# Kernel optimization log

Hardware: AMD Instinct MI355X
Metric: run time of the kernel (lower is better)

## Reference

```python
import jax, jax.numpy as jnp
import numpy as np

N = 100_000      # nodes
E = 1_600_000    # edges (avg degree 16)
F_IN = 128       # dataset.num_features
H = 128          # hidden
C = 25_000       # num_clusters (~ target_ratio 0.25 * N)
G = 64           # graphs in batch
NCLS = 10        # dataset.num_classes


def _gcn_conv(x, w, b, src, dst, n):
    # PyG GCNConv: add self loops, symmetric normalization deg^-1/2 A_hat deg^-1/2
    h = x @ w  # [n, out]
    deg = jnp.zeros((n,), x.dtype).at[dst].add(1.0) + 1.0  # +1 self loop
    dis = jax.lax.rsqrt(deg)
    norm = dis[src] * dis[dst]  # [E]
    out = jnp.zeros_like(h).at[dst].add(h[src] * norm[:, None])
    out = out + h * (dis * dis)[:, None]  # self-loop term norm_ii = deg_i^-1
    return out + b


def _mean_pool(x, seg, num_seg):
    s = jax.ops.segment_sum(x, seg, num_segments=num_seg)
    cnt = jax.ops.segment_sum(jnp.ones((x.shape[0],), x.dtype), seg, num_segments=num_seg)
    return s / jnp.maximum(cnt, 1.0)[:, None]


def _max_pool(x, seg, num_seg):
    m = jax.ops.segment_max(x, seg, num_segments=num_seg)
    cnt = jax.ops.segment_sum(jnp.ones((x.shape[0],), x.dtype), seg, num_segments=num_seg)
    return jnp.where(cnt[:, None] > 0, m, 0.0)


def setup_inputs() -> dict:
    key = jax.random.key(0)
    ks = jax.random.split(key, 12)
    def glorot(k, shape):
        fan_in = shape[0]
        return (jax.random.normal(k, shape, jnp.float32) / np.sqrt(fan_in)).astype(jnp.float32)
    return {
        "x": jax.random.normal(ks[0], (N, F_IN), jnp.float32),
        "edge_index": jax.random.randint(ks[1], (2, E), 0, N, dtype=jnp.int32).astype(jnp.int64),
        "batch": jnp.sort(jax.random.randint(ks[2], (N,), 0, G, dtype=jnp.int32)).astype(jnp.int64),
        "cluster": jax.random.randint(ks[3], (N,), 0, C, dtype=jnp.int32).astype(jnp.int64),
        "num_clusters": C,
        "num_graphs": G,
        "W1": glorot(ks[4], (F_IN, H)), "b1": jnp.zeros((H,), jnp.float32),
        "W2": glorot(ks[5], (H, H)),   "b2": jnp.zeros((H,), jnp.float32),
        "W3": glorot(ks[6], (H, H)),   "b3": jnp.zeros((H,), jnp.float32),
        "lin1_w": glorot(ks[7], (4 * H, H)), "lin1_b": jnp.zeros((H,), jnp.float32),
        "lin2_w": glorot(ks[8], (H, NCLS)),  "lin2_b": jnp.zeros((NCLS,), jnp.float32),
    }


def reference(x, edge_index, batch, cluster, num_clusters, num_graphs,
              W1, b1, W2, b2, W3, b3, lin1_w, lin1_b, lin2_w, lin2_b):
    n = x.shape[0]
    src, dst = edge_index[0], edge_index[1]
    # conv1 + relu (dropout is identity in eval mode)
    h = jax.nn.relu(_gcn_conv(x, W1, b1, src, dst, n))
    pre_mean = _mean_pool(h, batch, num_graphs)
    pre_max = _max_pool(h, batch, num_graphs)
    # LaCorePooling(aggregate='mean'): segment-mean nodes by cluster id,
    # relabel edges to cluster ids, derive pooled batch vector.
    hp = _mean_pool(h, cluster, num_clusters)            # [C, H]
    src_p, dst_p = cluster[src], cluster[dst]            # pooled edge list
    batch_p = jax.ops.segment_max(batch, cluster, num_segments=num_clusters)
    batch_p = jnp.maximum(batch_p, 0)                    # empty clusters -> graph 0
    # post-pool GCN layers
    hp = jax.nn.relu(_gcn_conv(hp, W2, b2, src_p, dst_p, num_clusters))
    hp = jax.nn.relu(_gcn_conv(hp, W3, b3, src_p, dst_p, num_clusters))
    post_mean = _mean_pool(hp, batch_p, num_graphs)
    post_max = _max_pool(hp, batch_p, num_graphs)
    z = jnp.concatenate([pre_mean, pre_max, post_mean, post_max], axis=-1)  # [G, 4H]
    z = jax.nn.relu(z @ lin1_w + lin1_b)
    z = z @ lin2_w + lin2_b
    return jax.nn.log_softmax(z, axis=-1)
```

## Files before the change

### kernel.cpp

```cpp
#include <hip/hip_runtime.h>

constexpr int N_NODES = 100000;
constexpr int N_EDGES = 1600000;
constexpr int N_CLUST = 25000;
constexpr int N_GRAPH = 64;
constexpr int NCLSN   = 10;

constexpr int BKT1_SHIFT = 9;
constexpr int NBKT1 = (N_NODES + 511) / 512;
constexpr int EPB = 4096;
constexpr int NEB = (N_EDGES + EPB - 1) / EPB;
constexpr int SORT_CAP = 12288;

constexpr int SCAN_BPB = 1024;
constexpr int NB1 = (N_NODES + SCAN_BPB - 1) / SCAN_BPB;
constexpr int NB2 = (N_CLUST + SCAN_BPB - 1) / SCAN_BPB;
constexpr int NB3 = (N_CLUST + SCAN_BPB - 1) / SCAN_BPB;
constexpr int NBT = NB1 + NB2 + NB3;

__device__ __forceinline__ float bf16lo(unsigned u){ return __uint_as_float(u << 16); }
__device__ __forceinline__ float bf16hi(unsigned u){ return __uint_as_float(u & 0xffff0000u); }
__device__ __forceinline__ unsigned bf16_rne(float f){
  unsigned u = __float_as_uint(f);
  return (u + 0x7fffu + ((u >> 16) & 1u)) >> 16;
}
__device__ __forceinline__ unsigned pack2(float lo, float hi){
  return bf16_rne(lo) | (bf16_rne(hi) << 16);
}

typedef short bf16x8 __attribute__((ext_vector_type(8)));
typedef float f32x4  __attribute__((ext_vector_type(4)));

__launch_bounds__(256)
__global__ void count_kernel(const int* __restrict__ ei, int* __restrict__ gcnt1){
  __shared__ int h1c[NBKT1];
  int t = threadIdx.x;
  for (int i = t; i < NBKT1; i += 256) h1c[i] = 0;
  __syncthreads();
  int e0 = blockIdx.x * EPB;
  #pragma unroll
  for (int i = 0; i < EPB / 256; ++i){
    int e = e0 + i * 256 + t;
    if (e < N_EDGES) atomicAdd(&h1c[ei[N_EDGES + e] >> BKT1_SHIFT], 1);
  }
  __syncthreads();
  for (int i = t; i < NBKT1; i += 256) if (h1c[i]) atomicAdd(&gcnt1[i], h1c[i]);
}

__launch_bounds__(256)
__global__ void bucket_scan(const int* __restrict__ gcnt1,
                            int* __restrict__ gbase1, int* __restrict__ gcur1){
  __shared__ int s[256];
  int t = threadIdx.x;
  int v = (t < NBKT1) ? gcnt1[t] : 0;
  s[t] = v; __syncthreads();
  for (int off = 1; off < 256; off <<= 1){
    int a = (t >= off) ? s[t - off] : 0;
    __syncthreads(); s[t] += a; __syncthreads();
  }
  if (t < NBKT1){ gbase1[t] = s[t] - v; gcur1[t] = s[t] - v; }
}

__launch_bounds__(256)
__global__ void scatter_kernel(const int* __restrict__ ei, int* __restrict__ gcur1,
                               unsigned int* __restrict__ stage1){
  __shared__ int h1c[NBKT1];
  __shared__ int gb1[NBKT1];
  int t = threadIdx.x;
  for (int i = t; i < NBKT1; i += 256) h1c[i] = 0;
  __syncthreads();
  int e0 = blockIdx.x * EPB;
  #pragma unroll
  for (int i = 0; i < EPB / 256; ++i){
    int e = e0 + i * 256 + t;
    if (e < N_EDGES) atomicAdd(&h1c[ei[N_EDGES + e] >> BKT1_SHIFT], 1);
  }
  __syncthreads();
  for (int i = t; i < NBKT1; i += 256){ int c = h1c[i]; gb1[i] = c ? atomicAdd(&gcur1[i], c) : 0; }
  __syncthreads();
  for (int i = t; i < NBKT1; i += 256) h1c[i] = 0;
  __syncthreads();
  #pragma unroll
  for (int i = 0; i < EPB / 256; ++i){
    int e = e0 + i * 256 + t;
    if (e < N_EDGES){
      int src = ei[e], dst = ei[N_EDGES + e];
      int b1 = dst >> BKT1_SHIFT;
      int r1 = atomicAdd(&h1c[b1], 1);
      stage1[gb1[b1] + r1] = ((unsigned)(dst & 511) << 17) | (unsigned)src;
    }
  }
}

template<int NBINS, int PSHIFT>
__launch_bounds__(256)
__global__ void bucket_sort(const unsigned int* __restrict__ stage, const int* __restrict__ gbase,
                            const int* __restrict__ gcnt, int* __restrict__ outpay,
                            int* __restrict__ deg, int ntot){
  __shared__ int cnt[NBINS], off[NBINS];
  __shared__ int sorted[SORT_CAP];
  int b = blockIdx.x, t = threadIdx.x;
  int base = gbase[b], n = gcnt[b];
  for (int i = t; i < NBINS; i += 256) cnt[i] = 0;
  __syncthreads();
  for (int i = t; i < n; i += 256) atomicAdd(&cnt[stage[base + i] >> PSHIFT], 1);
  __syncthreads();
  for (int i = t; i < NBINS; i += 256){
    int idx = b * NBINS + i;
    if (idx < ntot) deg[idx] = cnt[i];
    off[i] = cnt[i];
  }
  __syncthreads();
  for (int s = 1; s < NBINS; s <<= 1){
    int v0 = 0, v1 = 0;
    if (t < NBINS && t >= s) v0 = off[t - s];
    if (NBINS > 256 && t + 256 < NBINS && t + 256 >= s) v1 = off[t + 256 - s];
    __syncthreads();
    if (t < NBINS) off[t] += v0;
    if (NBINS > 256 && t + 256 < NBINS) off[t + 256] += v1;
    __syncthreads();
  }
  for (int i = t; i < NBINS; i += 256) off[i] -= cnt[i];
  __syncthreads();
  constexpr unsigned PMASK = (1u << PSHIFT) - 1u;
  if (n <= SORT_CAP){
    for (int i = t; i < n; i += 256){
      unsigned w = stage[base + i];
      int r = atomicAdd(&off[w >> PSHIFT], 1);
      sorted[r] = (int)(w & PMASK);
    }
    __syncthreads();
    for (int i = t; i < n; i += 256) outpay[base + i] = sorted[i];
  } else {
    for (int i = t; i < n; i += 256){
      unsigned w = stage[base + i];
      int r = atomicAdd(&off[w >> PSHIFT], 1);
      outpay[base + r] = (int)(w & PMASK);
    }
  }
}

__global__ void node_prep(const int* __restrict__ cluster, const int* __restrict__ deg1,
                          int* __restrict__ cntn, int* __restrict__ deg2){
  int v = blockIdx.x * blockDim.x + threadIdx.x;
  if (v < N_NODES){
    int c = cluster[v];
    atomicAdd(&cntn[c], 1);
    atomicAdd(&deg2[c], deg1[v]);
  }
}

__device__ __forceinline__ void seg_select(int b, const int* deg1, const int* cntn,
                                           const int* deg2, const int*& src, int& n, int& base){
  if (b < NB1){ src = deg1; n = N_NODES; base = b * SCAN_BPB; }
  else if (b < NB1 + NB2){ src = cntn; n = N_CLUST; base = (b - NB1) * SCAN_BPB; }
  else { src = deg2; n = N_CLUST; base = (b - NB1 - NB2) * SCAN_BPB; }
}

__launch_bounds__(256)
__global__ void block_sums(const int* __restrict__ deg1, const int* __restrict__ cntn,
                           const int* __restrict__ deg2, int* __restrict__ bsum){
  int b = blockIdx.x;
  const int* src; int n, base;
  seg_select(b, deg1, cntn, deg2, src, n, base);
  int t = threadIdx.x;
  int i0 = base + t * 4;
  int s = 0;
  if (i0 + 3 < n){ int4 v = *(const int4*)&src[i0]; s = v.x + v.y + v.z + v.w; }
  else { for (int j = 0; j < 4; ++j){ int i = i0 + j; if (i < n) s += src[i]; } }
  __shared__ int sh[256];
  sh[t] = s; __syncthreads();
  for (int off = 128; off > 0; off >>= 1){
    if (t < off) sh[t] += sh[t + off];
    __syncthreads();
  }
  if (t == 0) bsum[b] = sh[0];
}

__launch_bounds__(256)
__global__ void scan_bsums(const int* __restrict__ bsum, int* __restrict__ boff,
                           int* __restrict__ rowptr1, int* __restrict__ rowptrn,
                           int* __restrict__ rowptr2){
  __shared__ int s[256];
  int t = threadIdx.x;
  int v = (t < NBT) ? bsum[t] : 0;
  s[t] = v; __syncthreads();
  int seg = (t < NB1) ? 0 : (t < NB1 + NB2 ? 1 : 2);
  for (int off = 1; off < 256; off <<= 1){
    int add = 0;
    if (t >= off){
      int u = t - off;
      int useg = (u < NB1) ? 0 : (u < NB1 + NB2 ? 1 : 2);
      if (useg == seg) add = s[u];
    }
    __syncthreads();
    s[t] += add;
    __syncthreads();
  }
  if (t < NBT) boff[t] = s[t] - v;
  if (t == NB1 - 1)       rowptr1[N_NODES] = s[t];
  if (t == NB1 + NB2 - 1) rowptrn[N_CLUST] = s[t];
  if (t == NBT - 1)       rowptr2[N_CLUST] = s[t];
}

__launch_bounds__(256)
__global__ void scan_final(const int* __restrict__ deg1, const int* __restrict__ cntn,
                           const int* __restrict__ deg2, const int* __restrict__ boff,
                           int* __restrict__ rowptr1, float* __restrict__ dis1,
                           int* __restrict__ rowptrn, int* __restrict__ curn,
                           int* __restrict__ rowptr2, float* __restrict__ dis2){
  int b = blockIdx.x;
  const int* src; int n, base;
  seg_select(b, deg1, cntn, deg2, src, n, base);
  int* rp; int* cur; float* dis;
  if (b < NB1){ rp = rowptr1; cur = nullptr; dis = dis1; }
  else if (b < NB1 + NB2){ rp = rowptrn; cur = curn; dis = nullptr; }
  else { rp = rowptr2; cur = nullptr; dis = dis2; }
  int t = threadIdx.x;
  int i0 = base + t * 4;
  int v[4]; int s = 0;
  #pragma unroll
  for (int j = 0; j < 4; ++j){ int i = i0 + j; v[j] = (i < n) ? src[i] : 0; s += v[j]; }
  __shared__ int sh[256];
  sh[t] = s; __syncthreads();
  for (int off = 1; off < 256; off <<= 1){
    int add = (t >= off) ? sh[t - off] : 0;
    __syncthreads();
    sh[t] += add;
    __syncthreads();
  }
  int run = sh[t] - s + boff[b];
  #pragma unroll
  for (int j = 0; j < 4; ++j){
    int i = i0 + j;
    if (i < n){
      rp[i] = run;
      if (cur) cur[i] = run;
      if (dis) dis[i] = rsqrtf((float)v[j] + 1.0f);
      run += v[j];
    }
  }
}

__global__ void fill_n(const int* __restrict__ cluster, int* __restrict__ curn,
                       int* __restrict__ nidx){
  int v = blockIdx.x * blockDim.x + threadIdx.x;
  if (v >= N_NODES) return;
  nidx[atomicAdd(&curn[cluster[v]], 1)] = v;
}

__launch_bounds__(256)
__global__ void psrc_build(const int* __restrict__ rowptrn, const int* __restrict__ nidx,
                           const int* __restrict__ rowptr1, const int* __restrict__ esrc1,
                           const int* __restrict__ cluster, const int* __restrict__ rowptr2,
                           int* __restrict__ psrcC){
  int c = blockIdx.x * 4 + (threadIdx.x >> 6);
  int l = threadIdx.x & 63;
  int mb = rowptrn[c], me = rowptrn[c + 1];
  int cnt = me - mb;
  int base_l = 0, d_l = 0;
  if (l < cnt){
    int v = nidx[mb + l];
    base_l = rowptr1[v];
    d_l = rowptr1[v + 1] - base_l;
  }
  int pref = d_l;
  #pragma unroll
  for (int off = 1; off < 64; off <<= 1){
    int u = __shfl_up(pref, off);
    if (l >= off) pref += u;
  }
  int total = __shfl(pref, 63);
  int wbase = rowptr2[c];
  int iters = (total + 63) >> 6;
  for (int k = 0; k < iters; ++k){
    int idx = k * 64 + l;
    int idxc = min(idx, total - 1);
    int m = 0;
    for (int j = 0; j < cnt; ++j){
      int pj = __shfl(pref, j);
      if (idxc >= pj) m = j + 1;
    }
    int pm = __shfl(pref, m);
    int dm = __shfl(d_l, m);
    int bm = __shfl(base_l, m);
    int e = bm + idxc - (pm - dm);
    int sc = cluster[esrc1[e]];
    if (idx < total) psrcC[wbase + idx] = sc;
  }
}

template<bool A_BF16>
__launch_bounds__(256)
__global__ void gemm_mfma(const void* __restrict__ Aptr, const float* __restrict__ B,
                          const float* __restrict__ scale, unsigned* __restrict__ Cmat,
                          int M){
  __shared__ __align__(16) unsigned Blds[128 * 68];
  __shared__ __align__(16) unsigned Alds[64 * 68];
  const int t = threadIdx.x;
  const int row0 = blockIdx.x * 64;

  #pragma unroll
  for (int i = 0; i < 8; ++i){
    int task = t + i * 256;
    int kp = task >> 5, nq = task & 31;
    float4 b0 = *(const float4*)&B[(2 * kp) * 128 + nq * 4];
    float4 b1 = *(const float4*)&B[(2 * kp + 1) * 128 + nq * 4];
    Blds[(nq * 4 + 0) * 68 + kp] = pack2(b0.x, b1.x);
    Blds[(nq * 4 + 1) * 68 + kp] = pack2(b0.y, b1.y);
    Blds[(nq * 4 + 2) * 68 + kp] = pack2(b0.z, b1.z);
    Blds[(nq * 4 + 3) * 68 + kp] = pack2(b0.w, b1.w);
  }
  if (A_BF16){
    const unsigned* A = (const unsigned*)Aptr;
    #pragma unroll
    for (int i = 0; i < 8; ++i){
      int idx = t + i * 256;
      int row = idx >> 5, c2 = idx & 31;
      int grow = min(row0 + row, M - 1);
      uint2 v = *(const uint2*)&A[(size_t)grow * 64 + c2 * 2];
      Alds[row * 68 + c2 * 2]     = v.x;
      Alds[row * 68 + c2 * 2 + 1] = v.y;
    }
  } else {
    const float* A = (const float*)Aptr;
    #pragma unroll
    for (int i = 0; i < 8; ++i){
      int idx = t + i * 256;
      int row = idx >> 5, k4 = idx & 31;
      int grow = min(row0 + row, M - 1);
      float4 v = *(const float4*)&A[(size_t)grow * 128 + k4 * 4];
      Alds[row * 68 + k4 * 2]     = pack2(v.x, v.y);
      Alds[row * 68 + k4 * 2 + 1] = pack2(v.z, v.w);
    }
  }
  __syncthreads();

  const int wv = t >> 6, l = t & 63, quad = l >> 4, n16 = l & 15;
  f32x4 acc[8];
  #pragma unroll
  for (int nt = 0; nt < 8; ++nt) acc[nt] = (f32x4){0.f, 0.f, 0.f, 0.f};
  const int arow = wv * 16 + n16;
  #pragma unroll
  for (int ks = 0; ks < 4; ++ks){
    bf16x8 af = *(const bf16x8*)&Alds[arow * 68 + ks * 16 + quad * 4];
    #pragma unroll
    for (int nt = 0; nt < 8; ++nt){
      bf16x8 bfr = *(const bf16x8*)&Blds[(nt * 16 + n16) * 68 + ks * 16 + quad * 4];
      acc[nt] = __builtin_amdgcn_mfma_f32_16x16x32_bf16(af, bfr, acc[nt], 0, 0, 0);
    }
  }
  #pragma unroll
  for (int nt = 0; nt < 8; ++nt){
    #pragma unroll
    for (int r = 0; r < 4; ++r){
      int row = row0 + wv * 16 + quad * 4 + r;
      float sc = scale[min(row, M - 1)];
      float v = acc[nt][r] * sc;
      float vhi = __shfl_xor(v, 1);
      if (((l & 1) == 0) && row < M)
        Cmat[(size_t)row * 64 + nt * 8 + (n16 >> 1)] = pack2(v, vhi);
    }
  }
}

__launch_bounds__(256)
__global__ void conv_csr(const unsigned* __restrict__ Ts, const float* __restrict__ dis,
                         const int* __restrict__ rowptr, const int* __restrict__ esrc,
                         const float* __restrict__ bias, unsigned* __restrict__ Hout){
  int w = blockIdx.x * 4 + (threadIdx.x >> 6);
  int l = threadIdx.x & 63;
  int beg = rowptr[w], end = rowptr[w + 1];
  float2 a0{0.f,0.f}, a1{0.f,0.f}, a2{0.f,0.f}, a3{0.f,0.f};
  for (int base = beg; base < end; base += 64){
    int n = min(64, end - base);
    int eid = esrc[base + min(l, n - 1)];
    int j = 0;
    for (; j + 4 <= n; j += 4){
      int s0 = __shfl(eid, j);
      int s1 = __shfl(eid, j + 1);
      int s2 = __shfl(eid, j + 2);
      int s3 = __shfl(eid, j + 3);
      unsigned u0 = Ts[(size_t)s0 * 64 + l];
      unsigned u1 = Ts[(size_t)s1 * 64 + l];
      unsigned u2 = Ts[(size_t)s2 * 64 + l];
      unsigned u3 = Ts[(size_t)s3 * 64 + l];
      a0.x += bf16lo(u0); a0.y += bf16hi(u0);
      a1.x += bf16lo(u1); a1.y += bf16hi(u1);
      a2.x += bf16lo(u2); a2.y += bf16hi(u2);
      a3.x += bf16lo(u3); a3.y += bf16hi(u3);
    }
    for (; j < n; ++j){
      int s = __shfl(eid, j);
      unsigned u = Ts[(size_t)s * 64 + l];
      a0.x += bf16lo(u); a0.y += bf16hi(u);
    }
  }
  float d = dis[w];
  unsigned us = Ts[(size_t)w * 64 + l];
  float2 bb = *(const float2*)&bias[l * 2];
  float rx = fmaxf(fmaf(d, a0.x + a1.x + a2.x + a3.x + bf16lo(us), bb.x), 0.f);
  float ry = fmaxf(fmaf(d, a0.y + a1.y + a2.y + a3.y + bf16hi(us), bb.y), 0.f);
  Hout[(size_t)w * 64 + l] = pack2(rx, ry);
}

__launch_bounds__(256)
__global__ void cluster_gather(const unsigned* __restrict__ h1, const int* __restrict__ rowptrn,
                               const int* __restrict__ nidx, const int* __restrict__ batch,
                               unsigned* __restrict__ hp, int* __restrict__ batchp){
  int c = blockIdx.x * 4 + (threadIdx.x >> 6);
  int l = threadIdx.x & 63;
  int mb = rowptrn[c], me = rowptrn[c + 1];
  float2 a0{0.f,0.f}, a1{0.f,0.f}, a2{0.f,0.f}, a3{0.f,0.f};
  int vmax = -1;
  for (int base = mb; base < me; base += 64){
    int n = min(64, me - base);
    int vid = nidx[base + min(l, n - 1)];
    if (l < n) vmax = max(vmax, vid);
    int j = 0;
    for (; j + 4 <= n; j += 4){
      int s0 = __shfl(vid, j);
      int s1 = __shfl(vid, j + 1);
      int s2 = __shfl(vid, j + 2);
      int s3 = __shfl(vid, j + 3);
      unsigned u0 = h1[(size_t)s0 * 64 + l];
      unsigned u1 = h1[(size_t)s1 * 64 + l];
      unsigned u2 = h1[(size_t)s2 * 64 + l];
      unsigned u3 = h1[(size_t)s3 * 64 + l];
      a0.x += bf16lo(u0); a0.y += bf16hi(u0);
      a1.x += bf16lo(u1); a1.y += bf16hi(u1);
      a2.x += bf16lo(u2); a2.y += bf16hi(u2);
      a3.x += bf16lo(u3); a3.y += bf16hi(u3);
    }
    for (; j < n; ++j){
      int s = __shfl(vid, j);
      unsigned u = h1[(size_t)s * 64 + l];
      a0.x += bf16lo(u); a0.y += bf16hi(u);
    }
  }
  #pragma unroll
  for (int off = 32; off > 0; off >>= 1) vmax = max(vmax, __shfl_xor(vmax, off));
  float inv = 1.0f / (float)max(me - mb, 1);
  float ox = (a0.x + a1.x + a2.x + a3.x) * inv;
  float oy = (a0.y + a1.y + a2.y + a3.y) * inv;
  hp[(size_t)c * 64 + l] = pack2(ox, oy);
  if (l == 0) batchp[c] = (vmax >= 0) ? batch[vmax] : 0;
}

__global__ void cntp_kernel(const int* __restrict__ batchp, int* __restrict__ cntp){
  int c = blockIdx.x * blockDim.x + threadIdx.x;
  if (c < N_CLUST) atomicAdd(&cntp[batchp[c]], 1);
}

__global__ void scan_cntp(const int* __restrict__ cntp, int* __restrict__ gbasep,
                          int* __restrict__ curp){
  int t = threadIdx.x;
  int v = cntp[t];
  int s = v;
  for (int off = 1; off < 64; off <<= 1){
    int u = __shfl_up(s, off);
    if (t >= off) s += u;
  }
  gbasep[t] = s - v; curp[t] = s - v;
  if (t == 63) gbasep[64] = s;
}

__global__ void fill_c(const int* __restrict__ batchp, int* __restrict__ curp,
                       int* __restrict__ cidx){
  int c = blockIdx.x * blockDim.x + threadIdx.x;
  if (c < N_CLUST) cidx[atomicAdd(&curp[batchp[c]], 1)] = c;
}

__global__ void graph_bounds(const int* __restrict__ batch, int* __restrict__ gstart){
  int g = threadIdx.x;
  if (g > N_GRAPH) return;
  int lo = 0, hi = N_NODES;
  while (lo < hi){ int mid = (lo + hi) >> 1; if (batch[mid] < g) lo = mid + 1; else hi = mid; }
  gstart[g] = lo;
}

__device__ __forceinline__ void atomicMaxPosF(float* addr, float v){
  atomicMax((int*)addr, __float_as_int(v));
}

constexpr int PRE_SPLIT = 4;
__launch_bounds__(256)
__global__ void pre_pool_g(const unsigned* __restrict__ h1, const int* __restrict__ gstart,
                           float* __restrict__ psum, float* __restrict__ pmax){
  int g = blockIdx.x / PRE_SPLIT, sp = blockIdx.x % PRE_SPLIT;
  int t = threadIdx.x, w = t >> 6, l = t & 63;
  int s0 = gstart[g], s1 = gstart[g + 1];
  int n = s1 - s0;
  int per = (n + PRE_SPLIT - 1) / PRE_SPLIT;
  int b0 = s0 + sp * per, b1 = min(b0 + per, s1);
  float2 a0{0.f,0.f}, a1{0.f,0.f}, a2{0.f,0.f}, a3{0.f,0.f};
  float2 mx{0.f,0.f};
  int i = b0 + w;
  for (; i + 12 < b1; i += 16){
    unsigned u0 = h1[(size_t)(i     ) * 64 + l];
    unsigned u1 = h1[(size_t)(i +  4) * 64 + l];
    unsigned u2 = h1[(size_t)(i +  8) * 64 + l];
    unsigned u3 = h1[(size_t)(i + 12) * 64 + l];
    float f0x = bf16lo(u0), f0y = bf16hi(u0);
    float f1x = bf16lo(u1), f1y = bf16hi(u1);
    float f2x = bf16lo(u2), f2y = bf16hi(u2);
    float f3x = bf16lo(u3), f3y = bf16hi(u3);
    a0.x += f0x; a0.y += f0y; a1.x += f1x; a1.y += f1y;
    a2.x += f2x; a2.y += f2y; a3.x += f3x; a3.y += f3y;
    mx.x = fmaxf(fmaxf(mx.x, fmaxf(f0x, f1x)), fmaxf(f2x, f3x));
    mx.y = fmaxf(fmaxf(mx.y, fmaxf(f0y, f1y)), fmaxf(f2y, f3y));
  }
  for (; i < b1; i += 4){
    unsigned u = h1[(size_t)i * 64 + l];
    float fx = bf16lo(u), fy = bf16hi(u);
    a0.x += fx; a0.y += fy;
    mx.x = fmaxf(mx.x, fx); mx.y = fmaxf(mx.y, fy);
  }
  __shared__ float2 ssum[4][64], smax[4][64];
  ssum[w][l] = { a0.x + a1.x + a2.x + a3.x, a0.y + a1.y + a2.y + a3.y };
  smax[w][l] = mx;
  __syncthreads();
  if (w == 0){
    float2 S = ssum[0][l], M = smax[0][l];
    #pragma unroll
    for (int k = 1; k < 4; ++k){
      S.x += ssum[k][l].x; S.y += ssum[k][l].y;
      M.x = fmaxf(M.x, smax[k][l].x); M.y = fmaxf(M.y, smax[k][l].y);
    }
    atomicAdd(&psum[g * 128 + 2 * l], S.x);
    atomicAdd(&psum[g * 128 + 2 * l + 1], S.y);
    atomicMaxPosF(&pmax[g * 128 + 2 * l], M.x);
    atomicMaxPosF(&pmax[g * 128 + 2 * l + 1], M.y);
  }
}

constexpr int POST_SPLIT = 2;
__launch_bounds__(256)
__global__ void post_pool_g(const unsigned* __restrict__ hp3, const int* __restrict__ gbasep,
                            const int* __restrict__ cidx,
                            float* __restrict__ psum, float* __restrict__ pmax){
  int g = blockIdx.x / POST_SPLIT, sp = blockIdx.x % POST_SPLIT;
  int t = threadIdx.x, w = t >> 6, l = t & 63;
  int s0 = gbasep[g], s1 = gbasep[g + 1];
  int n = s1 - s0;
  int per = (n + POST_SPLIT * 4 - 1) / (POST_SPLIT * 4);
  int b0 = s0 + (sp * 4 + w) * per, b1 = min(b0 + per, s1);
  float2 a0{0.f,0.f}, a1{0.f,0.f}, a2{0.f,0.f}, a3{0.f,0.f};
  float2 mx{0.f,0.f};
  for (int base = b0; base < b1; base += 64){
    int nn = min(64, b1 - base);
    int cid = cidx[base + min(l, nn - 1)];
    int j = 0;
    for (; j + 4 <= nn; j += 4){
      int c0 = __shfl(cid, j);
      int c1 = __shfl(cid, j + 1);
      int c2 = __shfl(cid, j + 2);
      int c3 = __shfl(cid, j + 3);
      unsigned u0 = hp3[(size_t)c0 * 64 + l];
      unsigned u1 = hp3[(size_t)c1 * 64 + l];
      unsigned u2 = hp3[(size_t)c2 * 64 + l];
      unsigned u3 = hp3[(size_t)c3 * 64 + l];
      float f0x = bf16lo(u0), f0y = bf16hi(u0);
      float f1x = bf16lo(u1), f1y = bf16hi(u1);
      float f2x = bf16lo(u2), f2y = bf16hi(u2);
      float f3x = bf16lo(u3), f3y = bf16hi(u3);
      a0.x += f0x; a0.y += f0y; a1.x += f1x; a1.y += f1y;
      a2.x += f2x; a2.y += f2y; a3.x += f3x; a3.y += f3y;
      mx.x = fmaxf(fmaxf(mx.x, fmaxf(f0x, f1x)), fmaxf(f2x, f3x));
      mx.y = fmaxf(fmaxf(mx.y, fmaxf(f0y, f1y)), fmaxf(f2y, f3y));
    }
    for (; j < nn; ++j){
      int c = __shfl(cid, j);
      unsigned u = hp3[(size_t)c * 64 + l];
      float fx = bf16lo(u), fy = bf16hi(u);
      a0.x += fx; a0.y += fy;
      mx.x = fmaxf(mx.x, fx); mx.y = fmaxf(mx.y, fy);
    }
  }
  __shared__ float2 ssum[4][64], smax[4][64];
  ssum[w][l] = { a0.x + a1.x + a2.x + a3.x, a0.y + a1.y + a2.y + a3.y };
  smax[w][l] = mx;
  __syncthreads();
  if (w == 0){
    float2 S = ssum[0][l], M = smax[0][l];
    #pragma unroll
    for (int k = 1; k < 4; ++k){
      S.x += ssum[k][l].x; S.y += ssum[k][l].y;
      M.x = fmaxf(M.x, smax[k][l].x); M.y = fmaxf(M.y, smax[k][l].y);
    }
    atomicAdd(&psum[g * 128 + 2 * l], S.x);
    atomicAdd(&psum[g * 128 + 2 * l + 1], S.y);
    atomicMaxPosF(&pmax[g * 128 + 2 * l], M.x);
    atomicMaxPosF(&pmax[g * 128 + 2 * l + 1], M.y);
  }
}

__launch_bounds__(128)
__global__ void head_kernel(const float* __restrict__ psum, const float* __restrict__ pmax,
                            const float* __restrict__ postsum, const float* __restrict__ postmax,
                            const int* __restrict__ gstart, const int* __restrict__ cntp,
                            const float* __restrict__ l1w, const float* __restrict__ l1b,
                            const float* __restrict__ l2w, const float* __restrict__ l2b,
                            float* __restrict__ out){
  int g = blockIdx.x, t = threadIdx.x;
  __shared__ float z[512];
  __shared__ float a[128];
  __shared__ float logits[16];
  __shared__ float lse_s;
  float cpre  = (float)max(gstart[g + 1] - gstart[g], 1);
  float cpost = fmaxf((float)cntp[g], 1.0f);
  z[t]       = psum[g * 128 + t] / cpre;
  z[128 + t] = pmax[g * 128 + t];
  z[256 + t] = postsum[g * 128 + t] / cpost;
  z[384 + t] = postmax[g * 128 + t];
  __syncthreads();
  float acc = l1b[t];
  #pragma unroll 8
  for (int k = 0; k < 512; ++k) acc = fmaf(z[k], l1w[k * 128 + t], acc);
  a[t] = fmaxf(acc, 0.f);
  __syncthreads();
  if (t < NCLSN){
    float s2 = l2b[t];
    for (int k = 0; k < 128; ++k) s2 = fmaf(a[k], l2w[k * NCLSN + t], s2);
    logits[t] = s2;
  }
  __syncthreads();
  if (t == 0){
    float m = logits[0];
    for (int c = 1; c < NCLSN; ++c) m = fmaxf(m, logits[c]);
    float s = 0.f;
    for (int c = 0; c < NCLSN; ++c) s += expf(logits[c] - m);
    lse_s = m + logf(s);
  }
  __syncthreads();
  if (t < NCLSN) out[g * NCLSN + t] = logits[t] - lse_s;
}

extern "C" void kernel_launch(void* const* d_in, const int* in_sizes, int n_in,
                              void* d_out, int out_size, void* d_ws, size_t ws_size,
                              hipStream_t stream){
  const float* x       = (const float*)d_in[0];
  const int*   ei      = (const int*)  d_in[1];
  const int*   batch   = (const int*)  d_in[2];
  const int*   cluster = (const int*)  d_in[3];
  const float* W1      = (const float*)d_in[6];
  const float* b1      = (const float*)d_in[7];
  const float* W2      = (const float*)d_in[8];
  const float* b2      = (const float*)d_in[9];
  const float* W3      = (const float*)d_in[10];
  const float* b3      = (const float*)d_in[11];
  const float* l1w     = (const float*)d_in[12];
  const float* l1b     = (const float*)d_in[13];
  const float* l2w     = (const float*)d_in[14];
  const float* l2b     = (const float*)d_in[15];
  float* out = (float*)d_out;

  char* base = (char*)d_ws;
  size_t off = 0;
  auto alloc = [&](size_t bytes) -> char* {
    char* p = base + off;
    off += (bytes + 255) & ~size_t(255);
    return p;
  };
  char*  zbase  = base + off;
  int*   gcnt1  = (int*)  alloc((size_t)NBKT1 * 4);
  int*   cntn   = (int*)  alloc((size_t)N_CLUST * 4);
  int*   deg2   = (int*)  alloc((size_t)N_CLUST * 4);
  int*   cntp   = (int*)  alloc((size_t)N_GRAPH * 4);
  float* pre_s  = (float*)alloc((size_t)N_GRAPH * 128 * 4);
  float* pre_m  = (float*)alloc((size_t)N_GRAPH * 128 * 4);
  float* post_s = (float*)alloc((size_t)N_GRAPH * 128 * 4);
  float* post_m = (float*)alloc((size_t)N_GRAPH * 128 * 4);
  size_t zsize = off;
  unsigned* Ts1   = (unsigned*)alloc((size_t)N_NODES * 64 * 4);
  unsigned* h1    = (unsigned*)alloc((size_t)N_NODES * 64 * 4);
  int*   esrc1   = (int*)  alloc((size_t)N_EDGES * 4);
  int*   psrcC   = (int*)  alloc((size_t)N_EDGES * 4);
  int*   deg1    = (int*)  alloc((size_t)N_NODES * 4);
  int*   rowptr1 = (int*)  alloc((size_t)(N_NODES + 1) * 4);
  int*   rowptrn = (int*)  alloc((size_t)(N_CLUST + 1) * 4);
  int*   curn    = (int*)  alloc((size_t)N_CLUST * 4);
  int*   rowptr2 = (int*)  alloc((size_t)(N_CLUST + 1) * 4);
  int*   nidx    = (int*)  alloc((size_t)N_NODES * 4);
  float* dis1    = (float*)alloc((size_t)N_NODES * 4);
  float* dis2    = (float*)alloc((size_t)N_CLUST * 4);
  int*   batchp  = (int*)  alloc((size_t)N_CLUST * 4);
  int*   gstart  = (int*)  alloc((size_t)(N_GRAPH + 1) * 4);
  int*   bsum    = (int*)  alloc((size_t)NBT * 4);
  int*   boff    = (int*)  alloc((size_t)NBT * 4);
  int*   gbase1  = (int*)  alloc((size_t)NBKT1 * 4);
  int*   gcur1   = (int*)  alloc((size_t)NBKT1 * 4);
  int*   gbasep  = (int*)  alloc((size_t)(N_GRAPH + 1) * 4);
  int*   curp    = (int*)  alloc((size_t)N_GRAPH * 4);
  int*   cidx    = (int*)  alloc((size_t)N_CLUST * 4);
  unsigned int* stage1 = (unsigned int*)h1;
  unsigned* hp  = Ts1;
  unsigned* Ts2 = Ts1 + (size_t)N_CLUST * 64;
  unsigned* hp2 = Ts1 + (size_t)2 * N_CLUST * 64;
  unsigned* hp3 = Ts1 + (size_t)3 * N_CLUST * 64;
  unsigned* Ts3 = Ts2;

  (void)in_sizes; (void)n_in; (void)out_size; (void)ws_size;

  hipMemsetAsync(zbase, 0, zsize, stream);

  count_kernel  <<<NEB, 256, 0, stream>>>(ei, gcnt1);
  bucket_scan   <<<1, 256, 0, stream>>>(gcnt1, gbase1, gcur1);
  scatter_kernel<<<NEB, 256, 0, stream>>>(ei, gcur1, stage1);
  bucket_sort<512, 17><<<NBKT1, 256, 0, stream>>>(stage1, gbase1, gcnt1, esrc1, deg1, N_NODES);
  node_prep<<<(N_NODES + 255) / 256, 256, 0, stream>>>(cluster, deg1, cntn, deg2);
  block_sums <<<NBT, 256, 0, stream>>>(deg1, cntn, deg2, bsum);
  scan_bsums <<<1, 256, 0, stream>>>(bsum, boff, rowptr1, rowptrn, rowptr2);
  scan_final <<<NBT, 256, 0, stream>>>(deg1, cntn, deg2, boff,
                                       rowptr1, dis1, rowptrn, curn, rowptr2, dis2);
  fill_n<<<(N_NODES + 255) / 256, 256, 0, stream>>>(cluster, curn, nidx);
  psrc_build<<<N_CLUST / 4, 256, 0, stream>>>(rowptrn, nidx, rowptr1, esrc1,
                                              cluster, rowptr2, psrcC);

  gemm_mfma<false><<<(N_NODES + 63) / 64, 256, 0, stream>>>(x, W1, dis1, Ts1, N_NODES);
  conv_csr<<<N_NODES / 4, 256, 0, stream>>>(Ts1, dis1, rowptr1, esrc1, b1, h1);

  graph_bounds<<<1, 128, 0, stream>>>(batch, gstart);
  pre_pool_g<<<N_GRAPH * PRE_SPLIT, 256, 0, stream>>>(h1, gstart, pre_s, pre_m);

  cluster_gather<<<N_CLUST / 4, 256, 0, stream>>>(h1, rowptrn, nidx, batch, hp, batchp);
  cntp_kernel<<<(N_CLUST + 255) / 256, 256, 0, stream>>>(batchp, cntp);
  scan_cntp<<<1, 64, 0, stream>>>(cntp, gbasep, curp);
  fill_c<<<(N_CLUST + 255) / 256, 256, 0, stream>>>(batchp, curp, cidx);

  gemm_mfma<true><<<(N_CLUST + 63) / 64, 256, 0, stream>>>(hp, W2, dis2, Ts2, N_CLUST);
  conv_csr<<<N_CLUST / 4, 256, 0, stream>>>(Ts2, dis2, rowptr2, psrcC, b2, hp2);

  gemm_mfma<true><<<(N_CLUST + 63) / 64, 256, 0, stream>>>(hp2, W3, dis2, Ts3, N_CLUST);
  conv_csr<<<N_CLUST / 4, 256, 0, stream>>>(Ts3, dis2, rowptr2, psrcC, b3, hp3);

  post_pool_g<<<N_GRAPH * POST_SPLIT, 256, 0, stream>>>(hp3, gbasep, cidx, post_s, post_m);
  head_kernel<<<N_GRAPH, 128, 0, stream>>>(pre_s, pre_m, post_s, post_m, gstart, cntp,
                                           l1w, l1b, l2w, l2b, out);
}
```

Before: 608.0 us.

## Replace atomic bucket offsets with per-block histogram column scan; widen CSR unroll

The edge bucketing pipeline now stores per-block bucket histograms and computes per-block offsets with a column scan kernel. This replaces the global atomic cursor and lets the scatter kernel skip its recount pass. Count, scatter and sort kernels move to 1024-thread blocks. conv_csr gains an 8-way unrolled gather with eight accumulators for more memory-level parallelism, and the pre/post pooling split factors are doubled. The cost is an extra kernel launch and histogram buffers.

Result: faster. 536.3 us (-11.8%).

```diff
diff --git a/kernel.cpp b/kernel.cpp
--- a/kernel.cpp
+++ b/kernel.cpp
@@ -31,25 +31,40 @@
 typedef short bf16x8 __attribute__((ext_vector_type(8)));
 typedef float f32x4  __attribute__((ext_vector_type(4)));
 
-__launch_bounds__(256)
-__global__ void count_kernel(const int* __restrict__ ei, int* __restrict__ gcnt1){
+__launch_bounds__(1024)
+__global__ void count_kernel(const int* __restrict__ ei, int* __restrict__ bhist){
   __shared__ int h1c[NBKT1];
   int t = threadIdx.x;
-  for (int i = t; i < NBKT1; i += 256) h1c[i] = 0;
+  for (int i = t; i < NBKT1; i += 1024) h1c[i] = 0;
   __syncthreads();
   int e0 = blockIdx.x * EPB;
   #pragma unroll
-  for (int i = 0; i < EPB / 256; ++i){
-    int e = e0 + i * 256 + t;
+  for (int i = 0; i < EPB / 1024; ++i){
+    int e = e0 + i * 1024 + t;
     if (e < N_EDGES) atomicAdd(&h1c[ei[N_EDGES + e] >> BKT1_SHIFT], 1);
   }
   __syncthreads();
-  for (int i = t; i < NBKT1; i += 256) if (h1c[i]) atomicAdd(&gcnt1[i], h1c[i]);
-}
-
-__launch_bounds__(256)
-__global__ void bucket_scan(const int* __restrict__ gcnt1,
-                            int* __restrict__ gbase1, int* __restrict__ gcur1){
+  for (int i = t; i < NBKT1; i += 1024) bhist[blockIdx.x * NBKT1 + i] = h1c[i];
+}
+
+__launch_bounds__(512)
+__global__ void colscan(const int* __restrict__ bhist, int* __restrict__ boffs,
+                        int* __restrict__ gcnt1){
+  __shared__ int s[512];
+  int i = blockIdx.x;
+  int t = threadIdx.x;
+  int v = (t < NEB) ? bhist[t * NBKT1 + i] : 0;
+  s[t] = v; __syncthreads();
+  for (int o = 1; o < 512; o <<= 1){
+    int a = (t >= o) ? s[t - o] : 0;
+    __syncthreads(); s[t] += a; __syncthreads();
+  }
+  if (t < NEB) boffs[t * NBKT1 + i] = s[t] - v;
+  if (t == 511) gcnt1[i] = s[511];
+}
+
+__launch_bounds__(256)
+__global__ void bucket_scan(const int* __restrict__ gcnt1, int* __restrict__ gbase1){
   __shared__ int s[256];
   int t = threadIdx.x;
   int v = (t < NBKT1) ? gcnt1[t] : 0;
@@ -58,84 +73,73 @@
     int a = (t >= off) ? s[t - off] : 0;
     __syncthreads(); s[t] += a; __syncthreads();
   }
-  if (t < NBKT1){ gbase1[t] = s[t] - v; gcur1[t] = s[t] - v; }
-}
-
-__launch_bounds__(256)
-__global__ void scatter_kernel(const int* __restrict__ ei, int* __restrict__ gcur1,
-                               unsigned int* __restrict__ stage1){
-  __shared__ int h1c[NBKT1];
+  if (t < NBKT1) gbase1[t] = s[t] - v;
+}
+
+__launch_bounds__(1024)
+__global__ void scatter_kernel(const int* __restrict__ ei, const int* __restrict__ gbase1,
+                               const int* __restrict__ boffs, unsigned int* __restrict__ stage1){
   __shared__ int gb1[NBKT1];
-  int t = threadIdx.x;
-  for (int i = t; i < NBKT1; i += 256) h1c[i] = 0;
-  __syncthreads();
-  int e0 = blockIdx.x * EPB;
-  #pragma unroll
-  for (int i = 0; i < EPB / 256; ++i){
-    int e = e0 + i * 256 + t;
-    if (e < N_EDGES) atomicAdd(&h1c[ei[N_EDGES + e] >> BKT1_SHIFT], 1);
-  }
-  __syncthreads();
-  for (int i = t; i < NBKT1; i += 256){ int c = h1c[i]; gb1[i] = c ? atomicAdd(&gcur1[i], c) : 0; }
-  __syncthreads();
-  for (int i = t; i < NBKT1; i += 256) h1c[i] = 0;
-  __syncthreads();
-  #pragma unroll
-  for (int i = 0; i < EPB / 256; ++i){
-    int e = e0 + i * 256 + t;
+  __shared__ int cur[NBKT1];
+  int t = threadIdx.x, b = blockIdx.x;
+  for (int i = t; i < NBKT1; i += 1024){
+    gb1[i] = gbase1[i] + boffs[b * NBKT1 + i];
+    cur[i] = 0;
+  }
+  __syncthreads();
+  int e0 = b * EPB;
+  #pragma unroll
+  for (int i = 0; i < EPB / 1024; ++i){
+    int e = e0 + i * 1024 + t;
     if (e < N_EDGES){
       int src = ei[e], dst = ei[N_EDGES + e];
-      int b1 = dst >> BKT1_SHIFT;
-      int r1 = atomicAdd(&h1c[b1], 1);
-      stage1[gb1[b1] + r1] = ((unsigned)(dst & 511) << 17) | (unsigned)src;
-    }
-  }
-}
-
-template<int NBINS, int PSHIFT>
-__launch_bounds__(256)
+      int bk = dst >> BKT1_SHIFT;
+      int r = atomicAdd(&cur[bk], 1);
+      stage1[gb1[bk] + r] = ((unsigned)(dst & 511) << 17) | (unsigned)src;
+    }
+  }
+}
+
+__launch_bounds__(1024)
 __global__ void bucket_sort(const unsigned int* __restrict__ stage, const int* __restrict__ gbase,
                             const int* __restrict__ gcnt, int* __restrict__ outpay,
-                            int* __restrict__ deg, int ntot){
-  __shared__ int cnt[NBINS], off[NBINS];
+                            int* __restrict__ deg){
+  __shared__ int cnt[512], off[512];
   __shared__ int sorted[SORT_CAP];
   int b = blockIdx.x, t = threadIdx.x;
   int base = gbase[b], n = gcnt[b];
-  for (int i = t; i < NBINS; i += 256) cnt[i] = 0;
-  __syncthreads();
-  for (int i = t; i < n; i += 256) atomicAdd(&cnt[stage[base + i] >> PSHIFT], 1);
-  __syncthreads();
-  for (int i = t; i < NBINS; i += 256){
-    int idx = b * NBINS + i;
-    if (idx < ntot) deg[idx] = cnt[i];
-    off[i] = cnt[i];
-  }
-  __syncthreads();
-  for (int s = 1; s < NBINS; s <<= 1){
-    int v0 = 0, v1 = 0;
-    if (t < NBINS && t >= s) v0 = off[t - s];
-    if (NBINS > 256 && t + 256 < NBINS && t + 256 >= s) v1 = off[t + 256 - s];
+  if (t < 512) cnt[t] = 0;
+  __syncthreads();
+  for (int i = t; i < n; i += 1024) atomicAdd(&cnt[stage[base + i] >> 17], 1);
+  __syncthreads();
+  if (t < 512){
+    int idx = b * 512 + t;
+    if (idx < N_NODES) deg[idx] = cnt[t];
+    off[t] = cnt[t];
+  }
+  __syncthreads();
+  for (int s = 1; s < 512; s <<= 1){
+    int v = 0;
+    if (t < 512 && t >= s) v = off[t - s];
     __syncthreads();
-    if (t < NBINS) off[t] += v0;
-    if (NBINS > 256 && t + 256 < NBINS) off[t + 256] += v1;
+    if (t < 512) off[t] += v;
     __syncthreads();
   }
-  for (int i = t; i < NBINS; i += 256) off[i] -= cnt[i];
-  __syncthreads();
-  constexpr unsigned PMASK = (1u << PSHIFT) - 1u;
+  if (t < 512) off[t] -= cnt[t];
+  __syncthreads();
   if (n <= SORT_CAP){
-    for (int i = t; i < n; i += 256){
+    for (int i = t; i < n; i += 1024){
       unsigned w = stage[base + i];
-      int r = atomicAdd(&off[w >> PSHIFT], 1);
-      sorted[r] = (int)(w & PMASK);
+      int r = atomicAdd(&off[w >> 17], 1);
+      sorted[r] = (int)(w & 0x1FFFFu);
     }
     __syncthreads();
-    for (int i = t; i < n; i += 256) outpay[base + i] = sorted[i];
+    for (int i = t; i < n; i += 1024) outpay[base + i] = sorted[i];
   } else {
-    for (int i = t; i < n; i += 256){
+    for (int i = t; i < n; i += 1024){
       unsigned w = stage[base + i];
-      int r = atomicAdd(&off[w >> PSHIFT], 1);
-      outpay[base + r] = (int)(w & PMASK);
+      int r = atomicAdd(&off[w >> 17], 1);
+      outpay[base + r] = (int)(w & 0x1FFFFu);
     }
   }
 }
@@ -372,10 +376,37 @@
   int l = threadIdx.x & 63;
   int beg = rowptr[w], end = rowptr[w + 1];
   float2 a0{0.f,0.f}, a1{0.f,0.f}, a2{0.f,0.f}, a3{0.f,0.f};
+  float2 a4{0.f,0.f}, a5{0.f,0.f}, a6{0.f,0.f}, a7{0.f,0.f};
   for (int base = beg; base < end; base += 64){
     int n = min(64, end - base);
     int eid = esrc[base + min(l, n - 1)];
     int j = 0;
+    for (; j + 8 <= n; j += 8){
+      int s0 = __shfl(eid, j);
+      int s1 = __shfl(eid, j + 1);
+      int s2 = __shfl(eid, j + 2);
+      int s3 = __shfl(eid, j + 3);
+      int s4 = __shfl(eid, j + 4);
+      int s5 = __shfl(eid, j + 5);
+      int s6 = __shfl(eid, j + 6);
+      int s7 = __shfl(eid, j + 7);
+      unsigned u0 = Ts[(size_t)s0 * 64 + l];
+      unsigned u1 = Ts[(size_t)s1 * 64 + l];
+      unsigned u2 = Ts[(size_t)s2 * 64 + l];
+      unsigned u3 = Ts[(size_t)s3 * 64 + l];
+      unsigned u4 = Ts[(size_t)s4 * 64 + l];
+      unsigned u5 = Ts[(size_t)s5 * 64 + l];
+      unsigned u6 = Ts[(size_t)s6 * 64 + l];
+      unsigned u7 = Ts[(size_t)s7 * 64 + l];
+      a0.x += bf16lo(u0); a0.y += bf16hi(u0);
+      a1.x += bf16lo(u1); a1.y += bf16hi(u1);
+      a2.x += bf16lo(u2); a2.y += bf16hi(u2);
+      a3.x += bf16lo(u3); a3.y += bf16hi(u3);
+      a4.x += bf16lo(u4); a4.y += bf16hi(u4);
+      a5.x += bf16lo(u5); a5.y += bf16hi(u5);
+      a6.x += bf16lo(u6); a6.y += bf16hi(u6);
+      a7.x += bf16lo(u7); a7.y += bf16hi(u7);
+    }
     for (; j + 4 <= n; j += 4){
       int s0 = __shfl(eid, j);
       int s1 = __shfl(eid, j + 1);
@@ -399,8 +430,10 @@
   float d = dis[w];
   unsigned us = Ts[(size_t)w * 64 + l];
   float2 bb = *(const float2*)&bias[l * 2];
-  float rx = fmaxf(fmaf(d, a0.x + a1.x + a2.x + a3.x + bf16lo(us), bb.x), 0.f);
-  float ry = fmaxf(fmaf(d, a0.y + a1.y + a2.y + a3.y + bf16hi(us), bb.y), 0.f);
+  float sx = ((a0.x + a1.x) + (a2.x + a3.x)) + ((a4.x + a5.x) + (a6.x + a7.x)) + bf16lo(us);
+  float sy = ((a0.y + a1.y) + (a2.y + a3.y)) + ((a4.y + a5.y) + (a6.y + a7.y)) + bf16hi(us);
+  float rx = fmaxf(fmaf(d, sx, bb.x), 0.f);
+  float ry = fmaxf(fmaf(d, sy, bb.y), 0.f);
   Hout[(size_t)w * 64 + l] = pack2(rx, ry);
 }
 
@@ -483,7 +516,7 @@
   atomicMax((int*)addr, __float_as_int(v));
 }
 
-constexpr int PRE_SPLIT = 4;
+constexpr int PRE_SPLIT = 8;
 __launch_bounds__(256)
 __global__ void pre_pool_g(const unsigned* __restrict__ h1, const int* __restrict__ gstart,
                            float* __restrict__ psum, float* __restrict__ pmax){
@@ -534,7 +567,7 @@
   }
 }
 
-constexpr int POST_SPLIT = 2;
+constexpr int POST_SPLIT = 4;
 __launch_bounds__(256)
 __global__ void post_pool_g(const unsigned* __restrict__ hp3, const int* __restrict__ gbasep,
                             const int* __restrict__ cidx,
@@ -663,7 +696,6 @@
     return p;
   };
   char*  zbase  = base + off;
-  int*   gcnt1  = (int*)  alloc((size_t)NBKT1 * 4);
   int*   cntn   = (int*)  alloc((size_t)N_CLUST * 4);
   int*   deg2   = (int*)  alloc((size_t)N_CLUST * 4);
   int*   cntp   = (int*)  alloc((size_t)N_GRAPH * 4);
@@ -688,8 +720,10 @@
   int*   gstart  = (int*)  alloc((size_t)(N_GRAPH + 1) * 4);
   int*   bsum    = (int*)  alloc((size_t)NBT * 4);
   int*   boff    = (int*)  alloc((size_t)NBT * 4);
+  int*   gcnt1   = (int*)  alloc((size_t)NBKT1 * 4);
   int*   gbase1  = (int*)  alloc((size_t)NBKT1 * 4);
-  int*   gcur1   = (int*)  alloc((size_t)NBKT1 * 4);
+  int*   bhist   = (int*)  alloc((size_t)NEB * NBKT1 * 4);
+  int*   boffs   = (int*)  alloc((size_t)NEB * NBKT1 * 4);
   int*   gbasep  = (int*)  alloc((size_t)(N_GRAPH + 1) * 4);
   int*   curp    = (int*)  alloc((size_t)N_GRAPH * 4);
   int*   cidx    = (int*)  alloc((size_t)N_CLUST * 4);
@@ -704,10 +738,11 @@
 
   hipMemsetAsync(zbase, 0, zsize, stream);
 
-  count_kernel  <<<NEB, 256, 0, stream>>>(ei, gcnt1);
-  bucket_scan   <<<1, 256, 0, stream>>>(gcnt1, gbase1, gcur1);
-  scatter_kernel<<<NEB, 256, 0, stream>>>(ei, gcur1, stage1);
-  bucket_sort<512, 17><<<NBKT1, 256, 0, stream>>>(stage1, gbase1, gcnt1, esrc1, deg1, N_NODES);
+  count_kernel  <<<NEB, 1024, 0, stream>>>(ei, bhist);
+  colscan       <<<NBKT1, 512, 0, stream>>>(bhist, boffs, gcnt1);
+  bucket_scan   <<<1, 256, 0, stream>>>(gcnt1, gbase1);
+  scatter_kernel<<<NEB, 1024, 0, stream>>>(ei, gbase1, boffs, stage1);
+  bucket_sort   <<<NBKT1, 1024, 0, stream>>>(stage1, gbase1, gcnt1, esrc1, deg1);
   node_prep<<<(N_NODES + 255) / 256, 256, 0, stream>>>(cluster, deg1, cntn, deg2);
   block_sums <<<NBT, 256, 0, stream>>>(deg1, cntn, deg2, bsum);
   scan_bsums <<<1, 256, 0, stream>>>(bsum, boff, rowptr1, rowptrn, rowptr2);
```
